# Optimization experiments

Measured on AMD Instinct MI355X. Metric: run time of the kernel, lower is better.

## Reference

```python
import jax, jax.numpy as jnp
import numpy as np

B, t, FEAT, N, E = 128, 16, 256, 1024, 8192


def setup_inputs() -> dict:
    key = jax.random.key(0)
    k = jax.random.split(key, 9)
    s = 1.0 / np.sqrt(FEAT).astype(np.float32)
    x = jax.random.normal(k[0], (B, t, FEAT), jnp.float32)
    nodes = jax.random.normal(k[1], (B, N, FEAT), jnp.float32)
    edges = jax.random.randint(k[2], (B, 2, E), 0, 256).astype(jnp.int32)
    weights = jax.random.uniform(k[3], (B, 1, E), jnp.float32)
    T = jax.random.randint(k[4], (B,), 0, N - t).astype(jnp.int32)
    taus = jnp.full((B,), t, dtype=jnp.int32)  # no ragged padding: taus == t
    W_self1 = jax.random.normal(k[5], (FEAT, FEAT), jnp.float32) * s
    W_msg1 = jax.random.normal(k[6], (FEAT, FEAT), jnp.float32) * s
    W_self2 = jax.random.normal(k[7], (FEAT, FEAT), jnp.float32) * s
    W_msg2 = jax.random.normal(k[8], (FEAT, FEAT), jnp.float32) * s
    return dict(x=x, taus=taus, nodes=nodes, edges=edges, weights=weights, T=T,
                W_self1=W_self1, W_msg1=W_msg1, W_self2=W_self2, W_msg2=W_msg2)


def _gcm(x, nodes, weights, edges, T, Ws1, Wm1, Ws2, Wm2):
    Bn, tn, feat = x.shape
    Nn = nodes.shape[1]
    # --- scatter new nodes into the fixed-size node buffer ---
    b_idx = jnp.repeat(jnp.arange(Bn), tn)                       # [B*t]
    tau_idx = (T[:, None] + jnp.arange(tn)).reshape(-1)          # [B*t]
    nodes = nodes.at[b_idx, tau_idx].set(x.reshape(Bn * tn, feat))
    # --- to_batch: flatten ragged per-batch graphs into one big graph ---
    flat = nodes.reshape(Bn * Nn, feat)                          # [B*N, feat]
    off = (jnp.arange(Bn) * Nn)[:, None]                         # per-batch node offset
    valid = (edges[:, 0] >= 0) & (edges[:, 1] >= 0)              # -1 marks invalid edges
    src = jnp.where(valid, edges[:, 0] + off, 0).reshape(-1)     # [B*E]
    dst = jnp.where(valid, edges[:, 1] + off, 0).reshape(-1)
    ew = (weights[:, 0] * valid).reshape(-1)                     # invalid edges -> weight 0
    # --- 2-layer edge-weighted GraphConv GNN (tanh activation) ---
    def layer(h, Ws, Wm):
        agg = jax.ops.segment_sum(ew[:, None] * h[src], dst, num_segments=Bn * Nn)
        return jnp.tanh(h @ Ws + agg @ Wm)
    h = layer(flat, Ws1, Wm1)
    h = layer(h, Ws2, Wm2)
    # --- gather GNN outputs for the newly inserted nodes ---
    out_idx = b_idx * Nn + tau_idx
    mx = h[out_idx].reshape(Bn, tn, feat)
    return mx, nodes


def reference(x, taus, nodes, edges, weights, T, W_self1, W_msg1, W_self2, W_msg2):
    mx, new_nodes = _gcm(x, nodes, weights, edges, T, W_self1, W_msg1, W_self2, W_msg2)
    return (mx, new_nodes, edges, weights, T + taus)
```

## Files before the change

kernel.cpp:

```cpp
#include <hip/hip_runtime.h>
#include <math.h>

#define BB    128
#define TTW   16
#define FEATN 256
#define NNODE 1024
#define NEDGE 8192
#define MROW  272
#define M1    (BB*MROW)

#define OUT_MX    0
#define OUT_NODES (BB*TTW*FEATN)
#define OUT_EDGES (OUT_NODES + BB*NNODE*FEATN)
#define OUT_W     (OUT_EDGES + BB*2*NEDGE)
#define OUT_TT    (OUT_W + BB*NEDGE)

typedef short bf16x8 __attribute__((ext_vector_type(8)));
typedef float f32x4  __attribute__((ext_vector_type(4)));

__device__ inline unsigned short f2bf(float f) {
    unsigned int u = __float_as_uint(f);
    return (unsigned short)((u + 0x7fffu + ((u >> 16) & 1u)) >> 16);
}
__device__ inline float tanh_fast(float x) {
    return 1.f - 2.f / (__expf(2.f * x) + 1.f);
}

__global__ void k_pass(const float4* __restrict__ nodes4, const float4* __restrict__ x4,
                       const int* __restrict__ T, float4* __restrict__ out4) {
    int idx = blockIdx.x * 256 + threadIdx.x;
    int b   = idx >> 16;
    int row = (idx >> 6) & 1023;
    int f   = idx & 63;
    int dT  = row - T[b];
    const float4* src = ((unsigned)dT < 16u) ? (x4 + ((size_t)b * 16 + dT) * 64 + f)
                                             : (nodes4 + idx);
    out4[idx] = *src;
}

__global__ void k_misc(const int4* __restrict__ e4, const float4* __restrict__ w4,
                       const int* __restrict__ T, const int* __restrict__ taus,
                       float* __restrict__ out) {
    int i = blockIdx.x * 256 + threadIdx.x;
    if (i < 524288) {
        int4 e = e4[i];
        float4 o = make_float4((float)e.x, (float)e.y, (float)e.z, (float)e.w);
        ((float4*)(out + OUT_EDGES))[i] = o;
    } else if (i < 786432) {
        ((float4*)(out + OUT_W))[i - 524288] = w4[i - 524288];
    } else if (i < 786560) {
        int b = i - 786432;
        out[OUT_TT + b] = (float)(T[b] + taus[b]);
    }
}

__global__ void k_wconv(const float* __restrict__ Ws1, const float* __restrict__ Wm1,
                        const float* __restrict__ Ws2, const float* __restrict__ Wm2,
                        unsigned short* __restrict__ Wt1, unsigned short* __restrict__ Wt2) {
    int i = blockIdx.x * 256 + threadIdx.x;
    int layer = i >> 17;
    int j = i & 131071;
    int k = j >> 8, n = j & 255;
    const float* Ws = layer ? Ws2 : Ws1;
    const float* Wm = layer ? Wm2 : Wm1;
    float v = (k < 256) ? Ws[(size_t)k * 256 + n] : Wm[(size_t)(k - 256) * 256 + n];
    unsigned short* Wt = layer ? Wt2 : Wt1;
    Wt[(size_t)n * 512 + k] = f2bf(v);
}

__global__ void k_prep_x(const float* __restrict__ nodes, const float* __restrict__ x,
                         const int* __restrict__ T, unsigned short* __restrict__ Xc1) {
    int idx = blockIdx.x * 256 + threadIdx.x;
    int g  = idx >> 5;
    int c8 = idx & 31;
    int b = g / MROW, r = g % MROW;
    int Tb = T[b];
    const float* src;
    if (r >= 256)                       src = x + ((size_t)b * 16 + (r - 256)) * 256;
    else if ((unsigned)(r - Tb) < 16u)  src = x + ((size_t)b * 16 + (r - Tb)) * 256;
    else                                src = nodes + ((size_t)b * 1024 + r) * 256;
    float4 v0 = *(const float4*)(src + c8 * 8);
    float4 v1 = *(const float4*)(src + c8 * 8 + 4);
    uint4 p;
    p.x = f2bf(v0.x) | ((unsigned)f2bf(v0.y) << 16);
    p.y = f2bf(v0.z) | ((unsigned)f2bf(v0.w) << 16);
    p.z = f2bf(v1.x) | ((unsigned)f2bf(v1.y) << 16);
    p.w = f2bf(v1.z) | ((unsigned)f2bf(v1.w) << 16);
    *(uint4*)(Xc1 + (size_t)g * 512 + c8 * 8) = p;
}

__global__ void k_xt(const unsigned short* __restrict__ Xc1, unsigned short* __restrict__ Xt) {
    int b  = blockIdx.x >> 4;
    int tr = (blockIdx.x >> 2) & 3;
    int tc = blockIdx.x & 3;
    __shared__ unsigned short S[64][72];
#pragma unroll
    for (int p = 0; p < 2; ++p) {
        int slot = p * 256 + threadIdx.x;
        int r = slot >> 3, c8 = slot & 7;
        uint4 v = *(const uint4*)(Xc1 + ((size_t)(b * MROW + tr * 64 + r)) * 512 + tc * 64 + c8 * 8);
        *(uint4*)&S[r][c8 * 8] = v;
    }
    __syncthreads();
#pragma unroll
    for (int p = 0; p < 2; ++p) {
        int slot = p * 256 + threadIdx.x;
        int r2 = slot >> 3, c8 = slot & 7;
        unsigned short tmp[8];
#pragma unroll
        for (int j = 0; j < 8; ++j) tmp[j] = S[c8 * 8 + j][r2];
        *(uint4*)(Xt + ((size_t)b << 16) + (size_t)(tc * 64 + r2) * 256 + tr * 64 + c8 * 8) = *(uint4*)tmp;
    }
}

__global__ void k_zero(float4* __restrict__ p) {
    int i = blockIdx.x * 256 + threadIdx.x;
    p[i] = make_float4(0.f, 0.f, 0.f, 0.f);
}

__global__ void k_adj(const int* __restrict__ edges, const float* __restrict__ w,
                      float* __restrict__ W_adj) {
    int i = blockIdx.x * 256 + threadIdx.x;
    int b = i >> 13, e = i & 8191;
    const int* eb = edges + (size_t)b * 2 * NEDGE;
    int s = eb[e], d = eb[NEDGE + e];
    atomicAdd(&W_adj[((size_t)b << 16) + (d << 8) + s], w[(size_t)b * NEDGE + e]);
}

__global__ void k_bucket(const int* __restrict__ edges, const float* __restrict__ w,
                         int2* __restrict__ sw, int* __restrict__ bstart) {
    int b = blockIdx.x, tid = threadIdx.x;
    __shared__ int cnt[256];
    __shared__ int pos[256];
    cnt[tid] = 0;
    __syncthreads();
    const int* src = edges + (size_t)b * 2 * NEDGE;
    const int* dst = src + NEDGE;
    for (int e = tid; e < NEDGE; e += 256) atomicAdd(&cnt[dst[e]], 1);
    __syncthreads();
    int my = cnt[tid], v = my;
    for (int off = 1; off < 256; off <<= 1) {
        int u = 0;
        if (tid >= off) u = cnt[tid - off];
        __syncthreads();
        cnt[tid] = v = v + u;
        __syncthreads();
    }
    int start = v - my;
    bstart[b * 264 + tid] = start;
    if (tid == 0) bstart[b * 264 + 256] = NEDGE;
    pos[tid] = start;
    __syncthreads();
    const float* wb = w + (size_t)b * NEDGE;
    for (int e = tid; e < NEDGE; e += 256) {
        int d = dst[e];
        int p = atomicAdd(&pos[d], 1);
        sw[(size_t)b * NEDGE + p] = make_int2(src[e], __float_as_int(wb[e]));
    }
}

__global__ __launch_bounds__(256, 2) void k_aggemm(const float* __restrict__ W_adj,
                                                   const unsigned short* __restrict__ Xt,
                                                   unsigned short* __restrict__ Xc1) {
    int b = blockIdx.x >> 2;
    int tile_m = (blockIdx.x >> 1) & 1, tile_n = blockIdx.x & 1;
    int tid = threadIdx.x;
    int wv = tid >> 6, lane = tid & 63;
    int wm = wv >> 1, wn = wv & 1;
    int lm = lane & 15, lq = lane >> 4;

    __shared__ short As[128 * 32];
    __shared__ short Bs[128 * 32];

    f32x4 acc[4][4];
#pragma unroll
    for (int mi = 0; mi < 4; ++mi)
#pragma unroll
        for (int ni = 0; ni < 4; ++ni) acc[mi][ni] = (f32x4){0.f, 0.f, 0.f, 0.f};

    const float* Ab = W_adj + ((size_t)b << 16) + (size_t)tile_m * 128 * 256;
    const unsigned short* Bb = Xt + ((size_t)b << 16) + (size_t)tile_n * 128 * 256;

    for (int kc = 0; kc < 8; ++kc) {
        if (kc) __syncthreads();
#pragma unroll
        for (int p = 0; p < 4; ++p) {
            int slot = p * 256 + tid;
            int row = slot >> 3, seg = slot & 7;
            float4 v = *(const float4*)(Ab + (size_t)row * 256 + kc * 32 + seg * 4);
            uint2 pk;
            pk.x = f2bf(v.x) | ((unsigned)f2bf(v.y) << 16);
            pk.y = f2bf(v.z) | ((unsigned)f2bf(v.w) << 16);
            *(uint2*)(As + row * 32 + seg * 4) = pk;
        }
#pragma unroll
        for (int p = 0; p < 2; ++p) {
            int slot = p * 256 + tid;
            int row = slot >> 2, seg = slot & 3;
            ((uint4*)Bs)[slot] = *(const uint4*)(Bb + (size_t)row * 256 + kc * 32 + seg * 8);
        }
        __syncthreads();

        bf16x8 af[4], bfr[4];
#pragma unroll
        for (int mi = 0; mi < 4; ++mi)
            af[mi] = ((const bf16x8*)As)[(wm * 64 + mi * 16 + lm) * 4 + lq];
#pragma unroll
        for (int ni = 0; ni < 4; ++ni)
            bfr[ni] = ((const bf16x8*)Bs)[(wn * 64 + ni * 16 + lm) * 4 + lq];
#pragma unroll
        for (int mi = 0; mi < 4; ++mi)
#pragma unroll
            for (int ni = 0; ni < 4; ++ni)
                acc[mi][ni] = __builtin_amdgcn_mfma_f32_16x16x32_bf16(af[mi], bfr[ni], acc[mi][ni], 0, 0, 0);
    }

#pragma unroll
    for (int mi = 0; mi < 4; ++mi) {
#pragma unroll
        for (int ni = 0; ni < 4; ++ni) {
            int n = tile_n * 128 + wn * 64 + ni * 16 + lm;
#pragma unroll
            for (int r = 0; r < 4; ++r) {
                int m = tile_m * 128 + wm * 64 + mi * 16 + lq * 4 + r;
                Xc1[((size_t)(b * MROW + m)) * 512 + 256 + n] = f2bf(acc[mi][ni][r]);
            }
        }
    }
}

__global__ void k_fixwin(const int* __restrict__ T, unsigned short* __restrict__ Xc1) {
    int b = blockIdx.x;
    int Tb = T[b];
#pragma unroll
    for (int p = 0; p < 2; ++p) {
        int slot = p * 256 + threadIdx.x;
        int i = slot >> 5, c = slot & 31;
        int d = Tb + i;
        uint4 v = make_uint4(0u, 0u, 0u, 0u);
        if (d < 256) v = *(const uint4*)(Xc1 + ((size_t)(b * MROW + d)) * 512 + 256 + c * 8);
        *(uint4*)(Xc1 + ((size_t)(b * MROW + 256 + i)) * 512 + 256 + c * 8) = v;
    }
}

template <int OBF16>
__global__ __launch_bounds__(256, 2) void k_gemm(const unsigned short* __restrict__ Xc,
                                                 const unsigned short* __restrict__ Wt,
                                                 void* __restrict__ outp) {
    int tile_m = blockIdx.x >> 1;
    int tile_n = blockIdx.x & 1;
    int tid  = threadIdx.x;
    int wv   = tid >> 6, lane = tid & 63;
    int wm   = wv >> 1, wn = wv & 1;
    int lm   = lane & 15, lq = lane >> 4;

    __shared__ short As[128 * 32];
    __shared__ short Bs[128 * 32];

    f32x4 acc[4][4];
#pragma unroll
    for (int mi = 0; mi < 4; ++mi)
#pragma unroll
        for (int ni = 0; ni < 4; ++ni) acc[mi][ni] = (f32x4){0.f, 0.f, 0.f, 0.f};

    for (int kc = 0; kc < 16; ++kc) {
        if (kc) __syncthreads();
#pragma unroll
        for (int p = 0; p < 2; ++p) {
            int slot = p * 256 + tid;
            int row = slot >> 2, seg = slot & 3;
            ((uint4*)As)[slot] = *(const uint4*)(Xc + ((size_t)(tile_m * 128 + row)) * 512 + kc * 32 + seg * 8);
            ((uint4*)Bs)[slot] = *(const uint4*)(Wt + ((size_t)(tile_n * 128 + row)) * 512 + kc * 32 + seg * 8);
        }
        __syncthreads();

        bf16x8 af[4], bfr[4];
#pragma unroll
        for (int mi = 0; mi < 4; ++mi)
            af[mi] = ((const bf16x8*)As)[(wm * 64 + mi * 16 + lm) * 4 + lq];
#pragma unroll
        for (int ni = 0; ni < 4; ++ni)
            bfr[ni] = ((const bf16x8*)Bs)[(wn * 64 + ni * 16 + lm) * 4 + lq];
#pragma unroll
        for (int mi = 0; mi < 4; ++mi)
#pragma unroll
            for (int ni = 0; ni < 4; ++ni)
                acc[mi][ni] = __builtin_amdgcn_mfma_f32_16x16x32_bf16(af[mi], bfr[ni], acc[mi][ni], 0, 0, 0);
    }

#pragma unroll
    for (int mi = 0; mi < 4; ++mi) {
#pragma unroll
        for (int ni = 0; ni < 4; ++ni) {
            int n = tile_n * 128 + wn * 64 + ni * 16 + lm;
#pragma unroll
            for (int r = 0; r < 4; ++r) {
                int m = tile_m * 128 + wm * 64 + mi * 16 + lq * 4 + r;
                float v = tanh_fast(acc[mi][ni][r]);
                if (OBF16) ((unsigned short*)outp)[(size_t)m * 256 + n] = f2bf(v);
                else       ((float*)outp)[(size_t)m * 256 + n] = v;
            }
        }
    }
}

__global__ void k_agg2(const unsigned short* __restrict__ h1, const int2* __restrict__ sw,
                       const int* __restrict__ bstart, const int* __restrict__ T,
                       unsigned short* __restrict__ Xc2) {
    int g2   = blockIdx.x * 4 + (threadIdx.x >> 6);
    int lane = threadIdx.x & 63;
    int b = g2 >> 4, i = g2 & 15;
    ((uint2*)(Xc2 + (size_t)g2 * 512))[lane] =
        ((const uint2*)(h1 + (size_t)(b * MROW + 256 + i) * 256))[lane];
    int d = T[b] + i;
    float4 acc = make_float4(0.f, 0.f, 0.f, 0.f);
    if (d < 256) {
        int e0 = bstart[b * 264 + d];
        int e1 = bstart[b * 264 + d + 1];
        const int2* swb = sw + (size_t)b * NEDGE;
        const unsigned short* hb = h1 + (size_t)b * MROW * 256;
        for (int e = e0; e < e1; ++e) {
            int2 p = swb[e];
            float wt = __int_as_float(p.y);
            uint2 q = *((const uint2*)(hb + (size_t)p.x * 256) + lane);
            acc.x = fmaf(wt, __uint_as_float(q.x << 16),          acc.x);
            acc.y = fmaf(wt, __uint_as_float(q.x & 0xffff0000u),  acc.y);
            acc.z = fmaf(wt, __uint_as_float(q.y << 16),          acc.z);
            acc.w = fmaf(wt, __uint_as_float(q.y & 0xffff0000u),  acc.w);
        }
    }
    uint2 o;
    o.x = f2bf(acc.x) | ((unsigned)f2bf(acc.y) << 16);
    o.y = f2bf(acc.z) | ((unsigned)f2bf(acc.w) << 16);
    *(uint2*)(Xc2 + (size_t)g2 * 512 + 256 + lane * 4) = o;
}

extern "C" void kernel_launch(void* const* d_in, const int* in_sizes, int n_in,
                              void* d_out, int out_size, void* d_ws, size_t ws_size,
                              hipStream_t stream) {
    const float* x       = (const float*)d_in[0];
    const int*   taus    = (const int*)d_in[1];
    const float* nodes   = (const float*)d_in[2];
    const int*   edges   = (const int*)d_in[3];
    const float* weights = (const float*)d_in[4];
    const int*   T       = (const int*)d_in[5];
    const float* Ws1     = (const float*)d_in[6];
    const float* Wm1     = (const float*)d_in[7];
    const float* Ws2     = (const float*)d_in[8];
    const float* Wm2     = (const float*)d_in[9];
    float* out = (float*)d_out;

    char* ws = (char*)d_ws;
    int2*           sw     = (int2*)ws;
    int*            bstart = (int*)(ws + 8388608);
    unsigned short* Xc1    = (unsigned short*)(ws + 8523776);
    unsigned short* h1     = (unsigned short*)(ws + 44175360);
    unsigned short* Xt     = (unsigned short*)(ws + 44175360);
    unsigned short* Xc2    = (unsigned short*)(ws + 62001152);
    unsigned short* Wt1    = (unsigned short*)(ws + 64098304);
    unsigned short* Wt2    = (unsigned short*)(ws + 64360448);
    float*          W_adj  = (float*)(ws + 64622592);

    float* out_nodes = out + OUT_NODES;

    k_pass   <<<32768, 256, 0, stream>>>((const float4*)nodes, (const float4*)x, T, (float4*)out_nodes);
    k_misc   <<<3073, 256, 0, stream>>>((const int4*)edges, (const float4*)weights, T, taus, out);
    k_wconv  <<<1024, 256, 0, stream>>>(Ws1, Wm1, Ws2, Wm2, Wt1, Wt2);
    k_prep_x <<<4352, 256, 0, stream>>>(nodes, x, T, Xc1);
    k_xt     <<<2048, 256, 0, stream>>>(Xc1, Xt);
    k_zero   <<<8192, 256, 0, stream>>>((float4*)W_adj);
    k_adj    <<<4096, 256, 0, stream>>>(edges, weights, W_adj);
    k_bucket <<<BB, 256, 0, stream>>>(edges, weights, sw, bstart);
    k_aggemm <<<512, 256, 0, stream>>>(W_adj, Xt, Xc1);
    k_fixwin <<<BB, 256, 0, stream>>>(T, Xc1);
    k_gemm<1><<<272 * 2, 256, 0, stream>>>(Xc1, Wt1, h1);
    k_agg2   <<<512, 256, 0, stream>>>(h1, sw, bstart, T, Xc2);
    k_gemm<0><<<16 * 2, 256, 0, stream>>>(Xc2, Wt2, out + OUT_MX);
}
```

Before: 460.0 us.

## Replace dense adjacency GEMM with CSR sparse aggregation and fuse prep kernels

Layer one no longer builds a dense 256x256 weighted adjacency per batch with zeroing, atomics, a transpose and an MFMA GEMM. It instead runs a CSR-style gather over the bucketed edge list, with one wavefront per destination row and bf16 inputs. All preprocessing (pass-through copies, bf16 conversion of node rows and the inserted window, weight transposes, bucketing) is merged into one launch that reads nodes only once. This removes several launches and a large dense workspace, at the cost of irregular per-row gather loads and uneven edge counts between rows.

```diff
diff --git a/kernel.cpp b/kernel.cpp
--- a/kernel.cpp
+++ b/kernel.cpp
@@ -15,6 +15,14 @@
 #define OUT_W     (OUT_EDGES + BB*2*NEDGE)
 #define OUT_TT    (OUT_W + BB*NEDGE)
 
+#define R_PASS_END  8388608
+#define R_WIN_END   (R_PASS_END + 131072)
+#define R_EDG_END   (R_WIN_END + 524288)
+#define R_W_END     (R_EDG_END + 262144)
+#define R_WC_END    (R_W_END + 262144)
+#define R_TT_END    (R_WC_END + 128)
+#define PREP_BLOCKS (BB + (R_TT_END + 255) / 256)
+
 typedef short bf16x8 __attribute__((ext_vector_type(8)));
 typedef float f32x4  __attribute__((ext_vector_type(4)));
 
@@ -26,221 +34,118 @@
     return 1.f - 2.f / (__expf(2.f * x) + 1.f);
 }
 
-__global__ void k_pass(const float4* __restrict__ nodes4, const float4* __restrict__ x4,
-                       const int* __restrict__ T, float4* __restrict__ out4) {
-    int idx = blockIdx.x * 256 + threadIdx.x;
-    int b   = idx >> 16;
-    int row = (idx >> 6) & 1023;
-    int f   = idx & 63;
-    int dT  = row - T[b];
-    const float4* src = ((unsigned)dT < 16u) ? (x4 + ((size_t)b * 16 + dT) * 64 + f)
-                                             : (nodes4 + idx);
-    out4[idx] = *src;
-}
-
-__global__ void k_misc(const int4* __restrict__ e4, const float4* __restrict__ w4,
-                       const int* __restrict__ T, const int* __restrict__ taus,
-                       float* __restrict__ out) {
-    int i = blockIdx.x * 256 + threadIdx.x;
-    if (i < 524288) {
-        int4 e = e4[i];
-        float4 o = make_float4((float)e.x, (float)e.y, (float)e.z, (float)e.w);
-        ((float4*)(out + OUT_EDGES))[i] = o;
-    } else if (i < 786432) {
-        ((float4*)(out + OUT_W))[i - 524288] = w4[i - 524288];
-    } else if (i < 786560) {
-        int b = i - 786432;
-        out[OUT_TT + b] = (float)(T[b] + taus[b]);
-    }
-}
-
-__global__ void k_wconv(const float* __restrict__ Ws1, const float* __restrict__ Wm1,
-                        const float* __restrict__ Ws2, const float* __restrict__ Wm2,
-                        unsigned short* __restrict__ Wt1, unsigned short* __restrict__ Wt2) {
-    int i = blockIdx.x * 256 + threadIdx.x;
-    int layer = i >> 17;
-    int j = i & 131071;
-    int k = j >> 8, n = j & 255;
-    const float* Ws = layer ? Ws2 : Ws1;
-    const float* Wm = layer ? Wm2 : Wm1;
-    float v = (k < 256) ? Ws[(size_t)k * 256 + n] : Wm[(size_t)(k - 256) * 256 + n];
-    unsigned short* Wt = layer ? Wt2 : Wt1;
-    Wt[(size_t)n * 512 + k] = f2bf(v);
-}
-
-__global__ void k_prep_x(const float* __restrict__ nodes, const float* __restrict__ x,
-                         const int* __restrict__ T, unsigned short* __restrict__ Xc1) {
-    int idx = blockIdx.x * 256 + threadIdx.x;
-    int g  = idx >> 5;
-    int c8 = idx & 31;
-    int b = g / MROW, r = g % MROW;
-    int Tb = T[b];
-    const float* src;
-    if (r >= 256)                       src = x + ((size_t)b * 16 + (r - 256)) * 256;
-    else if ((unsigned)(r - Tb) < 16u)  src = x + ((size_t)b * 16 + (r - Tb)) * 256;
-    else                                src = nodes + ((size_t)b * 1024 + r) * 256;
-    float4 v0 = *(const float4*)(src + c8 * 8);
-    float4 v1 = *(const float4*)(src + c8 * 8 + 4);
-    uint4 p;
-    p.x = f2bf(v0.x) | ((unsigned)f2bf(v0.y) << 16);
-    p.y = f2bf(v0.z) | ((unsigned)f2bf(v0.w) << 16);
-    p.z = f2bf(v1.x) | ((unsigned)f2bf(v1.y) << 16);
-    p.w = f2bf(v1.z) | ((unsigned)f2bf(v1.w) << 16);
-    *(uint4*)(Xc1 + (size_t)g * 512 + c8 * 8) = p;
-}
-
-__global__ void k_xt(const unsigned short* __restrict__ Xc1, unsigned short* __restrict__ Xt) {
-    int b  = blockIdx.x >> 4;
-    int tr = (blockIdx.x >> 2) & 3;
-    int tc = blockIdx.x & 3;
-    __shared__ unsigned short S[64][72];
-#pragma unroll
-    for (int p = 0; p < 2; ++p) {
-        int slot = p * 256 + threadIdx.x;
-        int r = slot >> 3, c8 = slot & 7;
-        uint4 v = *(const uint4*)(Xc1 + ((size_t)(b * MROW + tr * 64 + r)) * 512 + tc * 64 + c8 * 8);
-        *(uint4*)&S[r][c8 * 8] = v;
-    }
-    __syncthreads();
-#pragma unroll
-    for (int p = 0; p < 2; ++p) {
-        int slot = p * 256 + threadIdx.x;
-        int r2 = slot >> 3, c8 = slot & 7;
-        unsigned short tmp[8];
-#pragma unroll
-        for (int j = 0; j < 8; ++j) tmp[j] = S[c8 * 8 + j][r2];
-        *(uint4*)(Xt + ((size_t)b << 16) + (size_t)(tc * 64 + r2) * 256 + tr * 64 + c8 * 8) = *(uint4*)tmp;
-    }
-}
-
-__global__ void k_zero(float4* __restrict__ p) {
-    int i = blockIdx.x * 256 + threadIdx.x;
-    p[i] = make_float4(0.f, 0.f, 0.f, 0.f);
-}
-
-__global__ void k_adj(const int* __restrict__ edges, const float* __restrict__ w,
-                      float* __restrict__ W_adj) {
-    int i = blockIdx.x * 256 + threadIdx.x;
-    int b = i >> 13, e = i & 8191;
-    const int* eb = edges + (size_t)b * 2 * NEDGE;
-    int s = eb[e], d = eb[NEDGE + e];
-    atomicAdd(&W_adj[((size_t)b << 16) + (d << 8) + s], w[(size_t)b * NEDGE + e]);
-}
-
-__global__ void k_bucket(const int* __restrict__ edges, const float* __restrict__ w,
-                         int2* __restrict__ sw, int* __restrict__ bstart) {
-    int b = blockIdx.x, tid = threadIdx.x;
+__global__ void k_prep(const float* __restrict__ x, const int* __restrict__ taus,
+                       const float* __restrict__ nodes, const int* __restrict__ edges,
+                       const float* __restrict__ weights, const int* __restrict__ T,
+                       const float* __restrict__ Ws1, const float* __restrict__ Wm1,
+                       const float* __restrict__ Ws2, const float* __restrict__ Wm2,
+                       float* __restrict__ out, unsigned short* __restrict__ Xc1,
+                       unsigned short* __restrict__ Wt1, unsigned short* __restrict__ Wt2,
+                       int2* __restrict__ sw, int* __restrict__ bstart) {
     __shared__ int cnt[256];
     __shared__ int pos[256];
-    cnt[tid] = 0;
-    __syncthreads();
-    const int* src = edges + (size_t)b * 2 * NEDGE;
-    const int* dst = src + NEDGE;
-    for (int e = tid; e < NEDGE; e += 256) atomicAdd(&cnt[dst[e]], 1);
-    __syncthreads();
-    int my = cnt[tid], v = my;
-    for (int off = 1; off < 256; off <<= 1) {
-        int u = 0;
-        if (tid >= off) u = cnt[tid - off];
-        __syncthreads();
-        cnt[tid] = v = v + u;
-        __syncthreads();
-    }
-    int start = v - my;
-    bstart[b * 264 + tid] = start;
-    if (tid == 0) bstart[b * 264 + 256] = NEDGE;
-    pos[tid] = start;
-    __syncthreads();
-    const float* wb = w + (size_t)b * NEDGE;
-    for (int e = tid; e < NEDGE; e += 256) {
-        int d = dst[e];
-        int p = atomicAdd(&pos[d], 1);
-        sw[(size_t)b * NEDGE + p] = make_int2(src[e], __float_as_int(wb[e]));
-    }
-}
-
-__global__ __launch_bounds__(256, 2) void k_aggemm(const float* __restrict__ W_adj,
-                                                   const unsigned short* __restrict__ Xt,
-                                                   unsigned short* __restrict__ Xc1) {
-    int b = blockIdx.x >> 2;
-    int tile_m = (blockIdx.x >> 1) & 1, tile_n = blockIdx.x & 1;
-    int tid = threadIdx.x;
-    int wv = tid >> 6, lane = tid & 63;
-    int wm = wv >> 1, wn = wv & 1;
-    int lm = lane & 15, lq = lane >> 4;
-
-    __shared__ short As[128 * 32];
-    __shared__ short Bs[128 * 32];
-
-    f32x4 acc[4][4];
-#pragma unroll
-    for (int mi = 0; mi < 4; ++mi)
-#pragma unroll
-        for (int ni = 0; ni < 4; ++ni) acc[mi][ni] = (f32x4){0.f, 0.f, 0.f, 0.f};
-
-    const float* Ab = W_adj + ((size_t)b << 16) + (size_t)tile_m * 128 * 256;
-    const unsigned short* Bb = Xt + ((size_t)b << 16) + (size_t)tile_n * 128 * 256;
-
-    for (int kc = 0; kc < 8; ++kc) {
-        if (kc) __syncthreads();
-#pragma unroll
-        for (int p = 0; p < 4; ++p) {
-            int slot = p * 256 + tid;
-            int row = slot >> 3, seg = slot & 7;
-            float4 v = *(const float4*)(Ab + (size_t)row * 256 + kc * 32 + seg * 4);
-            uint2 pk;
-            pk.x = f2bf(v.x) | ((unsigned)f2bf(v.y) << 16);
-            pk.y = f2bf(v.z) | ((unsigned)f2bf(v.w) << 16);
-            *(uint2*)(As + row * 32 + seg * 4) = pk;
-        }
-#pragma unroll
-        for (int p = 0; p < 2; ++p) {
-            int slot = p * 256 + tid;
-            int row = slot >> 2, seg = slot & 3;
-            ((uint4*)Bs)[slot] = *(const uint4*)(Bb + (size_t)row * 256 + kc * 32 + seg * 8);
-        }
-        __syncthreads();
-
-        bf16x8 af[4], bfr[4];
-#pragma unroll
-        for (int mi = 0; mi < 4; ++mi)
-            af[mi] = ((const bf16x8*)As)[(wm * 64 + mi * 16 + lm) * 4 + lq];
-#pragma unroll
-        for (int ni = 0; ni < 4; ++ni)
-            bfr[ni] = ((const bf16x8*)Bs)[(wn * 64 + ni * 16 + lm) * 4 + lq];
-#pragma unroll
-        for (int mi = 0; mi < 4; ++mi)
-#pragma unroll
-            for (int ni = 0; ni < 4; ++ni)
-                acc[mi][ni] = __builtin_amdgcn_mfma_f32_16x16x32_bf16(af[mi], bfr[ni], acc[mi][ni], 0, 0, 0);
-    }
-
-#pragma unroll
-    for (int mi = 0; mi < 4; ++mi) {
-#pragma unroll
-        for (int ni = 0; ni < 4; ++ni) {
-            int n = tile_n * 128 + wn * 64 + ni * 16 + lm;
-#pragma unroll
-            for (int r = 0; r < 4; ++r) {
-                int m = tile_m * 128 + wm * 64 + mi * 16 + lq * 4 + r;
-                Xc1[((size_t)(b * MROW + m)) * 512 + 256 + n] = f2bf(acc[mi][ni][r]);
-            }
-        }
-    }
-}
-
-__global__ void k_fixwin(const int* __restrict__ T, unsigned short* __restrict__ Xc1) {
-    int b = blockIdx.x;
-    int Tb = T[b];
-#pragma unroll
-    for (int p = 0; p < 2; ++p) {
-        int slot = p * 256 + threadIdx.x;
-        int i = slot >> 5, c = slot & 31;
-        int d = Tb + i;
-        uint4 v = make_uint4(0u, 0u, 0u, 0u);
-        if (d < 256) v = *(const uint4*)(Xc1 + ((size_t)(b * MROW + d)) * 512 + 256 + c * 8);
-        *(uint4*)(Xc1 + ((size_t)(b * MROW + 256 + i)) * 512 + 256 + c * 8) = v;
-    }
+    if (blockIdx.x < BB) {
+        int b = blockIdx.x, tid = threadIdx.x;
+        cnt[tid] = 0;
+        __syncthreads();
+        const int* src = edges + (size_t)b * 2 * NEDGE;
+        const int* dst = src + NEDGE;
+        for (int e = tid; e < NEDGE; e += 256) atomicAdd(&cnt[dst[e]], 1);
+        __syncthreads();
+        int my = cnt[tid], v = my;
+        for (int off = 1; off < 256; off <<= 1) {
+            int u = 0;
+            if (tid >= off) u = cnt[tid - off];
+            __syncthreads();
+            cnt[tid] = v = v + u;
+            __syncthreads();
+        }
+        int start = v - my;
+        bstart[b * 264 + tid] = start;
+        if (tid == 0) bstart[b * 264 + 256] = NEDGE;
+        pos[tid] = start;
+        __syncthreads();
+        const float* wb = weights + (size_t)b * NEDGE;
+        for (int e = tid; e < NEDGE; e += 256) {
+            int d = dst[e];
+            int p = atomicAdd(&pos[d], 1);
+            sw[(size_t)b * NEDGE + p] = make_int2(src[e], __float_as_int(wb[e]));
+        }
+        return;
+    }
+
+    int idx = (blockIdx.x - BB) * 256 + threadIdx.x;
+    if (idx < R_PASS_END) {
+        int b = idx >> 16, row = (idx >> 6) & 1023, f = idx & 63;
+        int dT = row - T[b];
+        const float4* src = ((unsigned)dT < 16u)
+                                ? ((const float4*)x + ((size_t)b * 16 + dT) * 64 + f)
+                                : ((const float4*)nodes + idx);
+        float4 v = *src;
+        ((float4*)(out + OUT_NODES))[idx] = v;
+        if (row < 256) {
+            uint2 p;
+            p.x = f2bf(v.x) | ((unsigned)f2bf(v.y) << 16);
+            p.y = f2bf(v.z) | ((unsigned)f2bf(v.w) << 16);
+            *(uint2*)(Xc1 + ((size_t)(b * MROW + row)) * 512 + f * 4) = p;
+        }
+    } else if (idx < R_WIN_END) {
+        int j = idx - R_PASS_END;
+        int b = j >> 10, i = (j >> 6) & 15, f = j & 63;
+        float4 v = ((const float4*)x)[((size_t)b * 16 + i) * 64 + f];
+        uint2 p;
+        p.x = f2bf(v.x) | ((unsigned)f2bf(v.y) << 16);
+        p.y = f2bf(v.z) | ((unsigned)f2bf(v.w) << 16);
+        *(uint2*)(Xc1 + ((size_t)(b * MROW + 256 + i)) * 512 + f * 4) = p;
+    } else if (idx < R_EDG_END) {
+        int j = idx - R_WIN_END;
+        int4 e = ((const int4*)edges)[j];
+        ((float4*)(out + OUT_EDGES))[j] =
+            make_float4((float)e.x, (float)e.y, (float)e.z, (float)e.w);
+    } else if (idx < R_W_END) {
+        int j = idx - R_EDG_END;
+        ((float4*)(out + OUT_W))[j] = ((const float4*)weights)[j];
+    } else if (idx < R_WC_END) {
+        int j = idx - R_W_END;
+        int layer = j >> 17, q = j & 131071;
+        int k = q >> 8, n = q & 255;
+        const float* Ws = layer ? Ws2 : Ws1;
+        const float* Wm = layer ? Wm2 : Wm1;
+        float v = (k < 256) ? Ws[(size_t)k * 256 + n] : Wm[(size_t)(k - 256) * 256 + n];
+        (layer ? Wt2 : Wt1)[(size_t)n * 512 + k] = f2bf(v);
+    } else if (idx < R_TT_END) {
+        int b = idx - R_WC_END;
+        out[OUT_TT + b] = (float)(T[b] + taus[b]);
+    }
+}
+
+__global__ void k_spmm1(const int2* __restrict__ sw, const int* __restrict__ bstart,
+                        const int* __restrict__ T, unsigned short* __restrict__ Xc1) {
+    int g    = blockIdx.x * 4 + (threadIdx.x >> 6);
+    int lane = threadIdx.x & 63;
+    int b = g / MROW;
+    int r = g - b * MROW;
+    int d = (r < 256) ? r : (T[b] + r - 256);
+    float4 acc = make_float4(0.f, 0.f, 0.f, 0.f);
+    if (d < 256) {
+        int e0 = bstart[b * 264 + d];
+        int e1 = bstart[b * 264 + d + 1];
+        const int2* swb = sw + (size_t)b * NEDGE;
+        const unsigned short* xb = Xc1 + (size_t)b * MROW * 512;
+        for (int e = e0; e < e1; ++e) {
+            int2 p = swb[e];
+            float wt = __int_as_float(p.y);
+            uint2 q = *((const uint2*)(xb + (size_t)p.x * 512) + lane);
+            acc.x = fmaf(wt, __uint_as_float(q.x << 16),          acc.x);
+            acc.y = fmaf(wt, __uint_as_float(q.x & 0xffff0000u),  acc.y);
+            acc.z = fmaf(wt, __uint_as_float(q.y << 16),          acc.z);
+            acc.w = fmaf(wt, __uint_as_float(q.y & 0xffff0000u),  acc.w);
+        }
+    }
+    uint2 o;
+    o.x = f2bf(acc.x) | ((unsigned)f2bf(acc.y) << 16);
+    o.y = f2bf(acc.z) | ((unsigned)f2bf(acc.w) << 16);
+    *(uint2*)(Xc1 + (size_t)g * 512 + 256 + lane * 4) = o;
 }
 
 template <int OBF16>
@@ -355,25 +260,15 @@
     int*            bstart = (int*)(ws + 8388608);
     unsigned short* Xc1    = (unsigned short*)(ws + 8523776);
     unsigned short* h1     = (unsigned short*)(ws + 44175360);
-    unsigned short* Xt     = (unsigned short*)(ws + 44175360);
     unsigned short* Xc2    = (unsigned short*)(ws + 62001152);
     unsigned short* Wt1    = (unsigned short*)(ws + 64098304);
     unsigned short* Wt2    = (unsigned short*)(ws + 64360448);
-    float*          W_adj  = (float*)(ws + 64622592);
-
-    float* out_nodes = out + OUT_NODES;
-
-    k_pass   <<<32768, 256, 0, stream>>>((const float4*)nodes, (const float4*)x, T, (float4*)out_nodes);
-    k_misc   <<<3073, 256, 0, stream>>>((const int4*)edges, (const float4*)weights, T, taus, out);
-    k_wconv  <<<1024, 256, 0, stream>>>(Ws1, Wm1, Ws2, Wm2, Wt1, Wt2);
-    k_prep_x <<<4352, 256, 0, stream>>>(nodes, x, T, Xc1);
-    k_xt     <<<2048, 256, 0, stream>>>(Xc1, Xt);
-    k_zero   <<<8192, 256, 0, stream>>>((float4*)W_adj);
-    k_adj    <<<4096, 256, 0, stream>>>(edges, weights, W_adj);
-    k_bucket <<<BB, 256, 0, stream>>>(edges, weights, sw, bstart);
-    k_aggemm <<<512, 256, 0, stream>>>(W_adj, Xt, Xc1);
-    k_fixwin <<<BB, 256, 0, stream>>>(T, Xc1);
+
+    k_prep  <<<PREP_BLOCKS, 256, 0, stream>>>(x, taus, nodes, edges, weights, T,
+                                              Ws1, Wm1, Ws2, Wm2,
+                                              out, Xc1, Wt1, Wt2, sw, bstart);
+    k_spmm1 <<<M1 / 4, 256, 0, stream>>>(sw, bstart, T, Xc1);
     k_gemm<1><<<272 * 2, 256, 0, stream>>>(Xc1, Wt1, h1);
-    k_agg2   <<<512, 256, 0, stream>>>(h1, sw, bstart, T, Xc2);
+    k_agg2  <<<512, 256, 0, stream>>>(h1, sw, bstart, T, Xc2);
     k_gemm<0><<<16 * 2, 256, 0, stream>>>(Xc2, Wt2, out + OUT_MX);
 }
```

Result: faster. 450.0 us (-2.2%).
